# Kernel tuning notes

Hardware: AMD Instinct MI355X
Metric: run time of the kernel (lower is better)

## Reference

```python
import jax, jax.numpy as jnp
import numpy as np

EMBED = 1024
HEADS = 16
HEAD_DIM = EMBED // HEADS


def setup_inputs() -> dict:
    key = jax.random.key(0)
    ks = jax.random.split(key, 9)
    N, L = 2, 2048
    values = jax.random.normal(ks[0], (N, L, EMBED), dtype=jnp.float32)
    keys = jax.random.normal(ks[1], (N, L, EMBED), dtype=jnp.float32)
    query = jax.random.normal(ks[2], (N, L, EMBED), dtype=jnp.float32)
    mask = jax.random.randint(ks[3], (N, 1, L, L), 0, 2, dtype=jnp.int32)
    s = 1.0 / np.sqrt(HEAD_DIM)
    Wv = jax.random.normal(ks[4], (HEAD_DIM, HEAD_DIM), dtype=jnp.float32) * s
    Wk = jax.random.normal(ks[5], (HEAD_DIM, HEAD_DIM), dtype=jnp.float32) * s
    Wq = jax.random.normal(ks[6], (HEAD_DIM, HEAD_DIM), dtype=jnp.float32) * s
    Wout = jax.random.normal(ks[7], (EMBED, EMBED), dtype=jnp.float32) * (1.0 / np.sqrt(EMBED))
    bout = jax.random.normal(ks[8], (EMBED,), dtype=jnp.float32) * 0.01
    return {"values": values, "keys": keys, "query": query, "mask": mask,
            "Wv": Wv, "Wk": Wk, "Wq": Wq, "Wout": Wout, "bout": bout}


def reference(values, keys, query, mask, Wv, Wk, Wq, Wout, bout):
    N, Lq, _ = query.shape
    Lk = keys.shape[1]
    # split heads: [N, L, H, D]
    v = values.reshape(N, Lk, HEADS, HEAD_DIM)
    k = keys.reshape(N, Lk, HEADS, HEAD_DIM)
    q = query.reshape(N, Lq, HEADS, HEAD_DIM)
    # per-head Linear (weight shared across heads), torch Linear: x @ W.T
    v = jnp.einsum('nlhd,ed->nlhe', v, Wv)
    k = jnp.einsum('nlhd,ed->nlhe', k, Wk)
    q = jnp.einsum('nlhd,ed->nlhe', q, Wq)
    # scores [N, H, Q, K]
    scores = jnp.einsum('nqhd,nkhd->nhqk', q, k)
    scores = jnp.where(mask == 0, jnp.float32(-1e20), scores)
    # NOTE: original scales by sqrt(embed_size), not sqrt(head_dim)
    attn = jax.nn.softmax(scores / jnp.sqrt(jnp.float32(EMBED)), axis=3)
    out = jnp.einsum('nhqk,nkhd->nqhd', attn, v).reshape(N, Lq, EMBED)
    return out @ Wout.T + bout
```

## Files before the change

### kernel.cpp

```cpp
#include <hip/hip_runtime.h>
#include <hip/hip_bf16.h>
#include <stdint.h>

typedef unsigned short u16;
typedef __attribute__((ext_vector_type(8))) short short8;
typedef __attribute__((ext_vector_type(4))) float float4_;

#define N_B   2
#define L_SEQ 2048
#define H_N   16
#define D_H   64
#define EMB   1024
#define KWORDS (L_SEQ/64)

#define C2 0.045084220027780106f

#define KP_OFF 0u
#define VP_OFF (8u*1024u*1024u)
#define X2_OFF (16u*1024u*1024u)
#define MP_OFF (24u*1024u*1024u)
#define WB_OFF (25u*1024u*1024u)

#define PREP_MASK  2048u
#define PREP_CVTW  (PREP_MASK + 512u)
#define PREP_PROJK (PREP_CVTW + 1024u)
#define PREP_TOTAL (PREP_PROJK + 1024u)

__device__ __forceinline__ u16 f2bf(float f) {
    __hip_bfloat16 h = __float2bfloat16(f);
    return *reinterpret_cast<u16*>(&h);
}
__device__ __forceinline__ short8 load8f(const float* p) {
    float4_ a = *(const float4_*)p;
    float4_ b = *(const float4_*)(p + 4);
    short8 r;
    r[0] = (short)f2bf(a[0]); r[1] = (short)f2bf(a[1]);
    r[2] = (short)f2bf(a[2]); r[3] = (short)f2bf(a[3]);
    r[4] = (short)f2bf(b[0]); r[5] = (short)f2bf(b[1]);
    r[6] = (short)f2bf(b[2]); r[7] = (short)f2bf(b[3]);
    return r;
}
__device__ __forceinline__ void gload16(const void* g, void* l) {
    __builtin_amdgcn_global_load_lds(
        (const __attribute__((address_space(1))) uint32_t*)(size_t)g,
        (__attribute__((address_space(3))) uint32_t*)(size_t)l, 16, 0, 0);
}
__device__ __forceinline__ uint32_t cvtpk(float a, float b) {
    uint32_t r;
    asm("v_cvt_pk_bf16_f32 %0, %1, %2" : "=v"(r) : "v"(a), "v"(b));
    return r;
}
__device__ __forceinline__ float fexp2(float x) {
    float r;
    asm("v_exp_f32 %0, %1" : "=v"(r) : "v"(x));
    return r;
}

__global__ __launch_bounds__(256) void prep_kernel(const int* __restrict__ mask,
                                                   unsigned long long* __restrict__ mp,
                                                   const float* __restrict__ Wout,
                                                   u16* __restrict__ wb,
                                                   const float* __restrict__ keys,
                                                   const float* __restrict__ Wk,
                                                   u16* __restrict__ kp,
                                                   const float* __restrict__ values,
                                                   const float* __restrict__ Wv,
                                                   u16* __restrict__ vpT) {
    unsigned bid = blockIdx.x;
    int tid = threadIdx.x;

    if (bid < PREP_MASK) {
        int lane = tid & 63;
        int wv   = tid >> 6;
        for (int j = 0; j < 16; j++) {
            int wid = bid * 64 + j * 4 + wv;
            int m = mask[(size_t)wid * 64 + lane];
            unsigned long long bits = __ballot(m != 0);
            if (lane == 0) mp[wid] = bits;
        }
        return;
    }
    if (bid < PREP_CVTW) {
        int i = ((bid - PREP_MASK) * 256 + tid) * 8;
        *(short8*)(wb + i) = load8f(Wout + i);
        return;
    }

    bool isK = bid < PREP_PROJK;
    unsigned lb = bid - (isK ? PREP_CVTW : PREP_PROJK);
    const float* x = isK ? keys : values;
    const float* W = isK ? Wk : Wv;

    int lt = lb & 31;
    int h  = (lb >> 5) & 15;
    int n  = lb >> 9;
    int w = tid >> 6, lane = tid & 63;
    int g = lane >> 4, r16 = lane & 15;
    int l0 = lt * 64 + w * 16;

    const float* xrow = x + ((size_t)(n * L_SEQ + l0 + r16)) * EMB + h * 64;
    short8 a0 = load8f(xrow + 8 * g);
    short8 a1 = load8f(xrow + 32 + 8 * g);

    short8 wf[4][2];
    for (int eb = 0; eb < 4; eb++)
        for (int ch = 0; ch < 2; ch++)
            wf[eb][ch] = load8f(W + (eb * 16 + r16) * 64 + ch * 32 + 8 * g);

    if (isK) {
        u16* ob = kp + ((size_t)((n * H_N + h) * L_SEQ + l0)) * 64;
        for (int eb = 0; eb < 4; eb++) {
            float4_ c = {0.f, 0.f, 0.f, 0.f};
            c = __builtin_amdgcn_mfma_f32_16x16x32_bf16(a0, wf[eb][0], c, 0, 0, 0);
            c = __builtin_amdgcn_mfma_f32_16x16x32_bf16(a1, wf[eb][1], c, 0, 0, 0);
            for (int i = 0; i < 4; i++)
                ob[(size_t)(4 * g + i) * 64 + eb * 16 + r16] = f2bf(c[i]);
        }
    } else {
        u16* obase = vpT + ((size_t)(n * H_N + h)) * (64 * L_SEQ) + l0 + r16;
        for (int eb = 0; eb < 4; eb++) {
            float4_ c = {0.f, 0.f, 0.f, 0.f};
            c = __builtin_amdgcn_mfma_f32_16x16x32_bf16(wf[eb][0], a0, c, 0, 0, 0);
            c = __builtin_amdgcn_mfma_f32_16x16x32_bf16(wf[eb][1], a1, c, 0, 0, 0);
            for (int i = 0; i < 4; i++)
                obase[(size_t)(eb * 16 + 4 * g + i) * L_SEQ] = f2bf(c[i]);
        }
    }
}

__global__ __launch_bounds__(256) void attn_kernel(const float* __restrict__ query,
                                                   const float* __restrict__ Wq,
                                                   const u16* __restrict__ kp,
                                                   const u16* __restrict__ vpT,
                                                   const unsigned long long* __restrict__ mp,
                                                   u16* __restrict__ x2) {
    __shared__ __align__(16) u16 Ks[2][64 * 64];
    __shared__ __align__(16) u16 Vt[2][64 * 64];
    __shared__ __align__(16) u16 Pt[4][16 * 64];

    int bid = blockIdx.x;
    int nh = bid & 31, qt = bid >> 5;
    int n = nh >> 4;
    int h = nh & 15;
    int tid = threadIdx.x;
    int w = tid >> 6, lane = tid & 63;
    int g = lane >> 4, r16 = lane & 15;
    int q0 = qt * 64 + w * 16;

    const u16* kb  = kp  + ((size_t)nh * L_SEQ) * 64;
    const u16* vtb = vpT + ((size_t)nh) * (64 * L_SEQ);

    int psw = (r16 & 7) << 4;

    {
        const float* qrow = query + ((size_t)(n * L_SEQ + q0 + r16)) * EMB + h * 64;
        short8 a0 = load8f(qrow + 8 * g);
        short8 a1 = load8f(qrow + 32 + 8 * g);
        for (int eb = 0; eb < 4; eb++) {
            short8 w0 = load8f(Wq + (eb * 16 + r16) * 64 + 8 * g);
            short8 w1 = load8f(Wq + (eb * 16 + r16) * 64 + 32 + 8 * g);
            float4_ c = {0.f, 0.f, 0.f, 0.f};
            c = __builtin_amdgcn_mfma_f32_16x16x32_bf16(a0, w0, c, 0, 0, 0);
            c = __builtin_amdgcn_mfma_f32_16x16x32_bf16(a1, w1, c, 0, 0, 0);
            for (int i = 0; i < 4; i++) {
                int row = 4 * g + i;
                *(u16*)((char*)Pt[w] + row * 128 + (((eb * 16 + r16) * 2) ^ ((row & 7) << 4))) = f2bf(c[i] * C2);
            }
        }
    }
    short8 aq0 = *(const short8*)((char*)Pt[w] + r16 * 128 + ((16 * g) ^ psw));
    short8 aq1 = *(const short8*)((char*)Pt[w] + r16 * 128 + ((64 + 16 * g) ^ psw));

    float4_ o[4] = {};
    float lpart = 0.f;
    const unsigned long long* mprow = mp + ((size_t)n * L_SEQ + q0 + r16) * KWORDS;

    int rs = (w << 3) + (lane >> 3);
    int cc = (lane & 7) ^ ((lane >> 3) & 7);

    #define STAGE(kt_, b_) do {                                                  \
        int k0_ = (kt_) * 64;                                                    \
        for (int h2 = 0; h2 < 2; h2++) {                                         \
            int r_ = rs + 32 * h2;                                               \
            gload16(kb  + (size_t)(k0_ + r_) * 64 + cc * 8,                      \
                    (char*)Ks[b_] + w * 1024 + h2 * 4096);                       \
            gload16(vtb + (size_t)r_ * L_SEQ + k0_ + cc * 8,                     \
                    (char*)Vt[b_] + w * 1024 + h2 * 4096);                       \
        }                                                                        \
    } while (0)

    STAGE(0, 0);
    int cur = 0;

    for (int kt = 0; kt < 32; kt++) {
        if (kt < 31) {
            STAGE(kt + 1, cur ^ 1);
            asm volatile("s_waitcnt vmcnt(4)" ::: "memory");
        } else {
            asm volatile("s_waitcnt vmcnt(0)" ::: "memory");
        }
        __builtin_amdgcn_sched_barrier(0);
        __builtin_amdgcn_s_barrier();
        __builtin_amdgcn_sched_barrier(0);

        unsigned long long word = mprow[kt];
        const char* ksb = (const char*)Ks[cur];
        const char* vtbuf = (const char*)Vt[cur];

        __builtin_amdgcn_s_setprio(1);
        for (int cb = 0; cb < 4; cb++) {
            int row = cb * 16 + r16;
            int sw = (row & 7) << 4;
            short8 bk0 = *(const short8*)(ksb + row * 128 + ((16 * g) ^ sw));
            short8 bk1 = *(const short8*)(ksb + row * 128 + ((64 + 16 * g) ^ sw));
            float4_ c = {0.f, 0.f, 0.f, 0.f};
            c = __builtin_amdgcn_mfma_f32_16x16x32_bf16(bk0, aq0, c, 0, 0, 0);
            c = __builtin_amdgcn_mfma_f32_16x16x32_bf16(bk1, aq1, c, 0, 0, 0);

            uint32_t nib = (uint32_t)(word >> (16 * cb + 4 * g)) & 0xFu;
            float p0 = (nib & 1u) ? fexp2(c[0]) : 0.f;
            float p1 = (nib & 2u) ? fexp2(c[1]) : 0.f;
            float p2 = (nib & 4u) ? fexp2(c[2]) : 0.f;
            float p3 = (nib & 8u) ? fexp2(c[3]) : 0.f;
            lpart += (p0 + p1) + (p2 + p3);
            uint2 pkv; pkv.x = cvtpk(p0, p1); pkv.y = cvtpk(p2, p3);
            *(uint2*)((char*)Pt[w] + r16 * 128 + ((cb * 32 + 8 * g) ^ psw)) = pkv;
        }

        short8 pb0 = *(const short8*)((char*)Pt[w] + r16 * 128 + ((16 * g) ^ psw));
        short8 pb1 = *(const short8*)((char*)Pt[w] + r16 * 128 + ((64 + 16 * g) ^ psw));

        for (int db = 0; db < 4; db++) {
            int row = db * 16 + r16;
            int sw = (row & 7) << 4;
            short8 av0 = *(const short8*)(vtbuf + row * 128 + ((16 * g) ^ sw));
            short8 av1 = *(const short8*)(vtbuf + row * 128 + ((64 + 16 * g) ^ sw));
            o[db] = __builtin_amdgcn_mfma_f32_16x16x32_bf16(av0, pb0, o[db], 0, 0, 0);
            o[db] = __builtin_amdgcn_mfma_f32_16x16x32_bf16(av1, pb1, o[db], 0, 0, 0);
        }
        __builtin_amdgcn_s_setprio(0);

        __builtin_amdgcn_sched_barrier(0);
        __builtin_amdgcn_s_barrier();
        cur ^= 1;
    }
    #undef STAGE

    float tot = lpart;
    tot += __shfl_xor(tot, 16);
    tot += __shfl_xor(tot, 32);
    float inv = 1.f / fmaxf(tot, 1e-30f);

    u16* ob = x2 + ((size_t)(n * L_SEQ + q0 + r16)) * EMB + h * 64;
    for (int db = 0; db < 4; db++)
        for (int i = 0; i < 4; i++)
            ob[db * 16 + 4 * g + i] = f2bf(o[db][i] * inv);
}

__global__ __launch_bounds__(512) void outgemm_kernel(const u16* __restrict__ x2,
                                                      const u16* __restrict__ Wb,
                                                      const float* __restrict__ bout,
                                                      float* __restrict__ out) {
    __shared__ __align__(16) u16 As[128 * 64];
    __shared__ __align__(16) u16 Bs[128 * 64];

    int bid = blockIdx.x;
    int mt = bid >> 3, nt = bid & 7;
    int m0 = mt * 128, n0 = nt * 128;
    int tid = threadIdx.x;
    int w = tid >> 6, lane = tid & 63;
    int g = lane >> 4, r16 = lane & 15;
    int wr = w >> 2, wc = w & 3;

    float4_ acc[4][2] = {};

    int rs = (w << 3) + (lane >> 3);
    int cc = (lane & 7) ^ ((lane >> 3) & 7);
    char* ldsA0 = (char*)As + w * 1024;
    char* ldsB0 = (char*)Bs + w * 1024;

    for (int kbk = 0; kbk < 16; kbk++) {
        int kk0 = kbk * 64;
        __syncthreads();
        for (int h2 = 0; h2 < 2; h2++) {
            int r = rs + 64 * h2;
            gload16(x2 + (size_t)(m0 + r) * EMB + kk0 + cc * 8, ldsA0 + h2 * 8192);
            gload16(Wb + (size_t)(n0 + r) * EMB + kk0 + cc * 8, ldsB0 + h2 * 8192);
        }
        __syncthreads();

        short8 afr[4][2], bfr[2][2];
        for (int sm = 0; sm < 4; sm++)
            for (int ch = 0; ch < 2; ch++) {
                int row = wr * 64 + sm * 16 + r16;
                afr[sm][ch] = *(const short8*)((char*)As + row * 128 + ((ch * 64 + 16 * g) ^ ((row & 7) << 4)));
            }
        for (int sn = 0; sn < 2; sn++)
            for (int ch = 0; ch < 2; ch++) {
                int row = wc * 32 + sn * 16 + r16;
                bfr[sn][ch] = *(const short8*)((char*)Bs + row * 128 + ((ch * 64 + 16 * g) ^ ((row & 7) << 4)));
            }
        for (int sm = 0; sm < 4; sm++)
            for (int sn = 0; sn < 2; sn++) {
                acc[sm][sn] = __builtin_amdgcn_mfma_f32_16x16x32_bf16(afr[sm][0], bfr[sn][0], acc[sm][sn], 0, 0, 0);
                acc[sm][sn] = __builtin_amdgcn_mfma_f32_16x16x32_bf16(afr[sm][1], bfr[sn][1], acc[sm][sn], 0, 0, 0);
            }
    }

    for (int sm = 0; sm < 4; sm++)
        for (int sn = 0; sn < 2; sn++) {
            int nn = n0 + wc * 32 + sn * 16 + r16;
            float bv = bout[nn];
            for (int i = 0; i < 4; i++) {
                int mm = m0 + wr * 64 + sm * 16 + 4 * g + i;
                out[(size_t)mm * EMB + nn] = acc[sm][sn][i] + bv;
            }
        }
}

extern "C" void kernel_launch(void* const* d_in, const int* in_sizes, int n_in,
                              void* d_out, int out_size, void* d_ws, size_t ws_size,
                              hipStream_t stream) {
    const float* values = (const float*)d_in[0];
    const float* keys   = (const float*)d_in[1];
    const float* query  = (const float*)d_in[2];
    const int*   mask   = (const int*)d_in[3];
    const float* Wv     = (const float*)d_in[4];
    const float* Wk     = (const float*)d_in[5];
    const float* Wq     = (const float*)d_in[6];
    const float* Wout   = (const float*)d_in[7];
    const float* bout   = (const float*)d_in[8];
    float* out = (float*)d_out;

    char* ws = (char*)d_ws;
    u16* kp  = (u16*)(ws + KP_OFF);
    u16* vpT = (u16*)(ws + VP_OFF);
    u16* x2  = (u16*)(ws + X2_OFF);
    unsigned long long* mpk = (unsigned long long*)(ws + MP_OFF);
    u16* wb  = (u16*)(ws + WB_OFF);

    prep_kernel<<<PREP_TOTAL, 256, 0, stream>>>(mask, mpk, Wout, wb,
                                                keys, Wk, kp, values, Wv, vpT);
    attn_kernel<<<1024, 256, 0, stream>>>(query, Wq, kp, vpT, mpk, x2);
    outgemm_kernel<<<256, 512, 0, stream>>>(x2, wb, bout, out);
}
```

Baseline: 232.6 us.

## Double-buffer output GEMM with smaller tiles and prefetch attention K/V earlier

The output projection GEMM moves from 128x128 tiles with 512 threads and synchronous loads to 64x64 tiles with 256 threads. It double-buffers LDS with async prefetch of the next K-slice, and launches 1024 blocks instead of 256 for better CU coverage. In the attention kernel, the first K/V tile load now starts before the Q projection, and the mask word load is issued ahead of the next stage's prefetch. The waitcnt is adjusted to account for the extra outstanding load. Smaller GEMM tiles lower per-block data reuse and increase global traffic in exchange for more parallelism and overlap.

```diff
diff --git a/kernel.cpp b/kernel.cpp
--- a/kernel.cpp
+++ b/kernel.cpp
@@ -151,6 +151,22 @@
     const u16* vtb = vpT + ((size_t)nh) * (64 * L_SEQ);
 
     int psw = (r16 & 7) << 4;
+
+    int rs = (w << 3) + (lane >> 3);
+    int cc = (lane & 7) ^ ((lane >> 3) & 7);
+
+    #define STAGE(kt_, b_) do {                                                  \
+        int k0_ = (kt_) * 64;                                                    \
+        for (int h2 = 0; h2 < 2; h2++) {                                         \
+            int r_ = rs + 32 * h2;                                               \
+            gload16(kb  + (size_t)(k0_ + r_) * 64 + cc * 8,                      \
+                    (char*)Ks[b_] + w * 1024 + h2 * 4096);                       \
+            gload16(vtb + (size_t)r_ * L_SEQ + k0_ + cc * 8,                     \
+                    (char*)Vt[b_] + w * 1024 + h2 * 4096);                       \
+        }                                                                        \
+    } while (0)
+
+    STAGE(0, 0);
 
     {
         const float* qrow = query + ((size_t)(n * L_SEQ + q0 + r16)) * EMB + h * 64;
@@ -175,36 +191,21 @@
     float lpart = 0.f;
     const unsigned long long* mprow = mp + ((size_t)n * L_SEQ + q0 + r16) * KWORDS;
 
-    int rs = (w << 3) + (lane >> 3);
-    int cc = (lane & 7) ^ ((lane >> 3) & 7);
-
-    #define STAGE(kt_, b_) do {                                                  \
-        int k0_ = (kt_) * 64;                                                    \
-        for (int h2 = 0; h2 < 2; h2++) {                                         \
-            int r_ = rs + 32 * h2;                                               \
-            gload16(kb  + (size_t)(k0_ + r_) * 64 + cc * 8,                      \
-                    (char*)Ks[b_] + w * 1024 + h2 * 4096);                       \
-            gload16(vtb + (size_t)r_ * L_SEQ + k0_ + cc * 8,                     \
-                    (char*)Vt[b_] + w * 1024 + h2 * 4096);                       \
-        }                                                                        \
-    } while (0)
-
-    STAGE(0, 0);
     int cur = 0;
-
     for (int kt = 0; kt < 32; kt++) {
+        unsigned long long word = mprow[kt];
+        __builtin_amdgcn_sched_barrier(0);
         if (kt < 31) {
             STAGE(kt + 1, cur ^ 1);
-            asm volatile("s_waitcnt vmcnt(4)" ::: "memory");
+            __builtin_amdgcn_sched_barrier(0);
+            asm volatile("s_waitcnt vmcnt(5)" ::: "memory");
         } else {
             asm volatile("s_waitcnt vmcnt(0)" ::: "memory");
         }
-        __builtin_amdgcn_sched_barrier(0);
         __builtin_amdgcn_s_barrier();
         __builtin_amdgcn_sched_barrier(0);
 
-        unsigned long long word = mprow[kt];
-        const char* ksb = (const char*)Ks[cur];
+        const char* ksb   = (const char*)Ks[cur];
         const char* vtbuf = (const char*)Vt[cur];
 
         __builtin_amdgcn_s_setprio(1);
@@ -257,62 +258,85 @@
             ob[db * 16 + 4 * g + i] = f2bf(o[db][i] * inv);
 }
 
-__global__ __launch_bounds__(512) void outgemm_kernel(const u16* __restrict__ x2,
+__global__ __launch_bounds__(256) void outgemm_kernel(const u16* __restrict__ x2,
                                                       const u16* __restrict__ Wb,
                                                       const float* __restrict__ bout,
                                                       float* __restrict__ out) {
-    __shared__ __align__(16) u16 As[128 * 64];
-    __shared__ __align__(16) u16 Bs[128 * 64];
+    __shared__ __align__(16) u16 As[2][64 * 64];
+    __shared__ __align__(16) u16 Bs[2][64 * 64];
 
     int bid = blockIdx.x;
-    int mt = bid >> 3, nt = bid & 7;
-    int m0 = mt * 128, n0 = nt * 128;
+    int mt = bid & 63, nt = bid >> 6;
+    int m0 = mt * 64, n0 = nt * 64;
     int tid = threadIdx.x;
     int w = tid >> 6, lane = tid & 63;
     int g = lane >> 4, r16 = lane & 15;
-    int wr = w >> 2, wc = w & 3;
-
-    float4_ acc[4][2] = {};
+    int wr = w >> 1, wc = w & 1;
+
+    float4_ acc[2][2] = {};
 
     int rs = (w << 3) + (lane >> 3);
     int cc = (lane & 7) ^ ((lane >> 3) & 7);
-    char* ldsA0 = (char*)As + w * 1024;
-    char* ldsB0 = (char*)Bs + w * 1024;
+
+    #define OSTAGE(kb_, b_) do {                                                 \
+        int kk_ = (kb_) * 64;                                                    \
+        for (int h2 = 0; h2 < 2; h2++) {                                         \
+            int r_ = rs + 32 * h2;                                               \
+            gload16(x2 + (size_t)(m0 + r_) * EMB + kk_ + cc * 8,                 \
+                    (char*)As[b_] + w * 1024 + h2 * 4096);                       \
+            gload16(Wb + (size_t)(n0 + r_) * EMB + kk_ + cc * 8,                 \
+                    (char*)Bs[b_] + w * 1024 + h2 * 4096);                       \
+        }                                                                        \
+    } while (0)
+
+    OSTAGE(0, 0);
+    int cur = 0;
 
     for (int kbk = 0; kbk < 16; kbk++) {
-        int kk0 = kbk * 64;
-        __syncthreads();
-        for (int h2 = 0; h2 < 2; h2++) {
-            int r = rs + 64 * h2;
-            gload16(x2 + (size_t)(m0 + r) * EMB + kk0 + cc * 8, ldsA0 + h2 * 8192);
-            gload16(Wb + (size_t)(n0 + r) * EMB + kk0 + cc * 8, ldsB0 + h2 * 8192);
-        }
-        __syncthreads();
-
-        short8 afr[4][2], bfr[2][2];
-        for (int sm = 0; sm < 4; sm++)
+        if (kbk < 15) {
+            OSTAGE(kbk + 1, cur ^ 1);
+            __builtin_amdgcn_sched_barrier(0);
+            asm volatile("s_waitcnt vmcnt(4)" ::: "memory");
+        } else {
+            asm volatile("s_waitcnt vmcnt(0)" ::: "memory");
+        }
+        __builtin_amdgcn_s_barrier();
+        __builtin_amdgcn_sched_barrier(0);
+
+        const char* pa = (const char*)As[cur];
+        const char* pb = (const char*)Bs[cur];
+
+        short8 afr[2][2], bfr[2][2];
+        for (int sm = 0; sm < 2; sm++)
             for (int ch = 0; ch < 2; ch++) {
-                int row = wr * 64 + sm * 16 + r16;
-                afr[sm][ch] = *(const short8*)((char*)As + row * 128 + ((ch * 64 + 16 * g) ^ ((row & 7) << 4)));
+                int row = wr * 32 + sm * 16 + r16;
+                afr[sm][ch] = *(const short8*)(pa + row * 128 + ((ch * 64 + 16 * g) ^ ((row & 7) << 4)));
             }
         for (int sn = 0; sn < 2; sn++)
             for (int ch = 0; ch < 2; ch++) {
                 int row = wc * 32 + sn * 16 + r16;
-                bfr[sn][ch] = *(const short8*)((char*)Bs + row * 128 + ((ch * 64 + 16 * g) ^ ((row & 7) << 4)));
-            }
-        for (int sm = 0; sm < 4; sm++)
+                bfr[sn][ch] = *(const short8*)(pb + row * 128 + ((ch * 64 + 16 * g) ^ ((row & 7) << 4)));
+            }
+        __builtin_amdgcn_s_setprio(1);
+        for (int sm = 0; sm < 2; sm++)
             for (int sn = 0; sn < 2; sn++) {
                 acc[sm][sn] = __builtin_amdgcn_mfma_f32_16x16x32_bf16(afr[sm][0], bfr[sn][0], acc[sm][sn], 0, 0, 0);
                 acc[sm][sn] = __builtin_amdgcn_mfma_f32_16x16x32_bf16(afr[sm][1], bfr[sn][1], acc[sm][sn], 0, 0, 0);
             }
-    }
-
-    for (int sm = 0; sm < 4; sm++)
+        __builtin_amdgcn_s_setprio(0);
+
+        __builtin_amdgcn_sched_barrier(0);
+        __builtin_amdgcn_s_barrier();
+        cur ^= 1;
+    }
+    #undef OSTAGE
+
+    for (int sm = 0; sm < 2; sm++)
         for (int sn = 0; sn < 2; sn++) {
             int nn = n0 + wc * 32 + sn * 16 + r16;
             float bv = bout[nn];
             for (int i = 0; i < 4; i++) {
-                int mm = m0 + wr * 64 + sm * 16 + 4 * g + i;
+                int mm = m0 + wr * 32 + sm * 16 + 4 * g + i;
                 out[(size_t)mm * EMB + nn] = acc[sm][sn][i] + bv;
             }
         }
@@ -342,5 +366,5 @@
     prep_kernel<<<PREP_TOTAL, 256, 0, stream>>>(mask, mpk, Wout, wb,
                                                 keys, Wk, kp, values, Wv, vpT);
     attn_kernel<<<1024, 256, 0, stream>>>(query, Wq, kp, vpT, mpk, x2);
-    outgemm_kernel<<<256, 512, 0, stream>>>(x2, wb, bout, out);
-}
+    outgemm_kernel<<<1024, 256, 0, stream>>>(x2, wb, bout, out);
+}
```

Result: no change. 230.1 us (-1.1%).
